# Optimization experiments

Measured on AMD Instinct MI355X. Metric: run time of the kernel, lower is better.

## Reference

```python
import jax, jax.numpy as jnp
import numpy as np

POOLSCALE = 4  # HSA: avg-pool kernel/stride = (scale, scale*4)

def _avg_pool(x, kh, kw):
    # kernel == stride and dims divisible -> exact reshape-mean pooling
    B, C, H, W = x.shape
    return x.reshape(B, C, H // kh, kh, W // kw, kw).mean(axis=(3, 5))

def setup_inputs() -> dict:
    key = jax.random.key(0)
    k1, k2, k3 = jax.random.split(key, 3)
    shape = (4, 64, 192, 192)
    return {
        "K": jax.random.normal(k1, shape, dtype=jnp.float32),
        "Q": jax.random.normal(k2, shape, dtype=jnp.float32),
        "V": jax.random.normal(k3, shape, dtype=jnp.float32),
    }

def reference(K, Q, V):
    B, C, H, W = Q.shape
    kh, kw = POOLSCALE, POOLSCALE * 4
    Qp = Q.reshape(B, C, H * W).transpose(0, 2, 1)          # [B, HW, C]
    Kp = _avg_pool(K, kh, kw)                               # [B, C, h, w]
    Kp = Kp.reshape(B, C, -1)                               # [B, C, hw_p]
    Vp = _avg_pool(V, kh, kw).reshape(B, C, -1)             # [B, C, hw_p]
    scores = jnp.einsum('bnc,bcm->bnm', Qp, Kp)             # [B, HW, hw_p]
    attn = jax.nn.softmax(scores, axis=1)                   # softmax over query dim (dim=1), as in torch code
    out = jnp.einsum('bcm,bnm->bcn', Vp, attn)              # V_pie @ attn^T -> [B, C, HW]
    return out.reshape(B, C, H, W)
```

## Files before the change

kernel.cpp:

```cpp
#include <hip/hip_runtime.h>
#include <stdint.h>

#define BB 4
#define CC 64
#define HH 192
#define WW 192
#define HWN (HH*WW)
#define KH 4
#define KW 16
#define PW (WW/KW)
#define MP ((HH/KH)*(WW/KW))
#define MITER (MP/64)
#define NCHUNK (HWN/256)
#define NBTOT (HWN/32)
#define SCALE_W 65536.0f
#define INV_SCALE (1.0f/65536.0f)

typedef _Float16 half8 __attribute__((ext_vector_type(8)));
typedef _Float16 half4 __attribute__((ext_vector_type(4)));
typedef float floatx4 __attribute__((ext_vector_type(4)));

static __device__ __forceinline__ void gload16(const void* g, void* l) {
  __builtin_amdgcn_global_load_lds((const __attribute__((address_space(1))) void*)g,
                                   (__attribute__((address_space(3))) void*)l, 16, 0, 0);
}
#define WAITCNT_VM(N) asm volatile("s_waitcnt vmcnt(" #N ")" ::: "memory")
#define WAITCNT_LGKM0 asm volatile("s_waitcnt lgkmcnt(0)" ::: "memory")


__global__ __launch_bounds__(256) void pool_kernel(
    const float* __restrict__ Kin, const float* __restrict__ Vin,
    _Float16* __restrict__ kptF, float* __restrict__ vp) {
  int t = blockIdx.x * 256 + threadIdx.x;
  const int total = BB * CC * MP;
  bool isV = t >= total;
  int idx = isV ? t - total : t;
  int m = idx % MP;
  int c = (idx / MP) % CC;
  int b = idx / (MP * CC);
  int mh = m / PW, mw = m % PW;
  const float* src = (isV ? Vin : Kin) + (((b * CC + c) * HH + mh * KH) * WW + mw * KW);
  float s = 0.f;
#pragma unroll
  for (int r = 0; r < KH; ++r) {
    const float4* row = (const float4*)(src + r * WW);
#pragma unroll
    for (int j = 0; j < KW / 4; ++j) {
      float4 v = row[j];
      s += v.x + v.y + v.z + v.w;
    }
  }
  s *= (1.0f / (KH * KW));
  if (isV) {
    vp[(b * CC + c) * MP + m] = s;
  } else {
    int mi = m >> 6, mloc = m & 63, l15 = mloc >> 2, mf = mloc & 3;
    int ks = c >> 5, lhi = (c >> 3) & 3, e = c & 7;
    int lane = lhi * 16 + l15;
    kptF[(((((b * MITER + mi) * 4 + mf) * 2 + ks)) * 64 + lane) * 8 + e] = (_Float16)s;
  }
}

__global__ __launch_bounds__(256) void qprep_kernel(
    const float* __restrict__ Q, _Float16* __restrict__ qF) {
  int t = blockIdx.x * 256 + threadIdx.x;
  int chunk = t >> 6;
  int lane = t & 63;
  int nf = chunk & 1;
  int ks = (chunk >> 1) & 1;
  int idx = chunk >> 2;
  int nb = idx % NBTOT;
  int b = idx / NBTOT;
  int c0 = ks * 32 + (lane >> 4) * 8;
  int n = nb * 32 + nf * 16 + (lane & 15);
  const float* Qb = Q + (b * CC + c0) * HWN + n;
  half8 h;
#pragma unroll
  for (int e = 0; e < 8; ++e) h[e] = (_Float16)Qb[e * HWN];
  *(half8*)(qF + chunk * 512 + lane * 8) = h;
}

__global__ __launch_bounds__(512) void colsum_qf_kernel(
    const _Float16* __restrict__ qF, const _Float16* __restrict__ kptF,
    float* __restrict__ part) {
  int tid = threadIdx.x;
  int lane = tid & 63;
  int l15 = lane & 15;
  int u = blockIdx.x * 8 + (tid >> 6);
  int mi = u % 9;
  int v = u / 9;
  int b = v / NCHUNK;
  int nc = v % NCHUNK;

  const _Float16* kb = kptF + b * MITER * 8 * 512;
  half8 bfr[4][2];
#pragma unroll
  for (int mf = 0; mf < 4; ++mf)
#pragma unroll
    for (int ks = 0; ks < 2; ++ks)
      bfr[mf][ks] = *(const half8*)(kb + ((mi * 4 + mf) * 2 + ks) * 512 + lane * 8);

  floatx4 zero = {0.f, 0.f, 0.f, 0.f};
  float s0 = 0.f, s1 = 0.f, s2 = 0.f, s3 = 0.f;

#pragma unroll
  for (int it = 0; it < 8; ++it) {
    int nb = nc * 8 + it;
    const _Float16* qc = qF + (size_t)((b * NBTOT + nb) * 4) * 512 + lane * 8;
    half8 af[2][2];
#pragma unroll
    for (int ks = 0; ks < 2; ++ks)
#pragma unroll
      for (int nf = 0; nf < 2; ++nf)
        af[nf][ks] = *(const half8*)(qc + (ks * 2 + nf) * 512);

    floatx4 sacc[2][4];
#pragma unroll
    for (int nf = 0; nf < 2; ++nf)
#pragma unroll
      for (int mf = 0; mf < 4; ++mf) sacc[nf][mf] = zero;
    __builtin_amdgcn_s_setprio(1);
#pragma unroll
    for (int ks = 0; ks < 2; ++ks)
#pragma unroll
      for (int nf = 0; nf < 2; ++nf)
#pragma unroll
        for (int mf = 0; mf < 4; ++mf)
          sacc[nf][mf] = __builtin_amdgcn_mfma_f32_16x16x32_f16(
              af[nf][ks], bfr[mf][ks], sacc[nf][mf], 0, 0, 0);
    __builtin_amdgcn_s_setprio(0);

#pragma unroll
    for (int nf = 0; nf < 2; ++nf)
#pragma unroll
      for (int r = 0; r < 4; ++r) {
        s0 += __expf(sacc[nf][0][r]);
        s1 += __expf(sacc[nf][1][r]);
        s2 += __expf(sacc[nf][2][r]);
        s3 += __expf(sacc[nf][3][r]);
      }
  }

  s0 += __shfl_xor(s0, 16); s0 += __shfl_xor(s0, 32);
  s1 += __shfl_xor(s1, 16); s1 += __shfl_xor(s1, 32);
  s2 += __shfl_xor(s2, 16); s2 += __shfl_xor(s2, 32);
  s3 += __shfl_xor(s3, 16); s3 += __shfl_xor(s3, 32);
  if (lane < 16) {
    float* p = part + (b * NCHUNK + nc) * MP + mi * 64 + l15 * 4;
    p[0] = s0; p[1] = s1; p[2] = s2; p[3] = s3;
  }
}

__global__ __launch_bounds__(576) void colsum_fb_kernel(
    const float* __restrict__ Q, const _Float16* __restrict__ kptF,
    float* __restrict__ part) {
  int b = blockIdx.y;
  int n0 = blockIdx.x * 256;
  int tid = threadIdx.x;
  int wv = tid / 64;
  int lane = tid & 63;
  int l15 = lane & 15, lhi = lane >> 4;

  const _Float16* kb = kptF + b * MITER * 8 * 512;
  half8 bfr[4][2];
#pragma unroll
  for (int mf = 0; mf < 4; ++mf)
#pragma unroll
    for (int ks = 0; ks < 2; ++ks)
      bfr[mf][ks] = *(const half8*)(kb + ((wv * 4 + mf) * 2 + ks) * 512 + lane * 8);

  const float* Qb = Q + b * CC * HWN;
  floatx4 zero = {0.f, 0.f, 0.f, 0.f};
  float s0 = 0.f, s1 = 0.f, s2 = 0.f, s3 = 0.f;

#pragma unroll
  for (int it = 0; it < 8; ++it) {
    int nr = n0 + it * 32 + l15;
    half8 af[2][2];
#pragma unroll
    for (int nf = 0; nf < 2; ++nf)
#pragma unroll
      for (int ks = 0; ks < 2; ++ks)
#pragma unroll
        for (int e = 0; e < 8; ++e)
          af[nf][ks][e] = (_Float16)Qb[(ks * 32 + lhi * 8 + e) * HWN + nr + nf * 16];

    floatx4 sacc[2][4];
#pragma unroll
    for (int nf = 0; nf < 2; ++nf)
#pragma unroll
      for (int mf = 0; mf < 4; ++mf) sacc[nf][mf] = zero;
    __builtin_amdgcn_s_setprio(1);
#pragma unroll
    for (int ks = 0; ks < 2; ++ks)
#pragma unroll
      for (int nf = 0; nf < 2; ++nf)
#pragma unroll
        for (int mf = 0; mf < 4; ++mf)
          sacc[nf][mf] = __builtin_amdgcn_mfma_f32_16x16x32_f16(
              af[nf][ks], bfr[mf][ks], sacc[nf][mf], 0, 0, 0);
    __builtin_amdgcn_s_setprio(0);

#pragma unroll
    for (int nf = 0; nf < 2; ++nf)
#pragma unroll
      for (int r = 0; r < 4; ++r) {
        s0 += __expf(sacc[nf][0][r]);
        s1 += __expf(sacc[nf][1][r]);
        s2 += __expf(sacc[nf][2][r]);
        s3 += __expf(sacc[nf][3][r]);
      }
  }

  s0 += __shfl_xor(s0, 16); s0 += __shfl_xor(s0, 32);
  s1 += __shfl_xor(s1, 16); s1 += __shfl_xor(s1, 32);
  s2 += __shfl_xor(s2, 16); s2 += __shfl_xor(s2, 32);
  s3 += __shfl_xor(s3, 16); s3 += __shfl_xor(s3, 32);
  if (lane < 16) {
    float* p = part + (b * NCHUNK + blockIdx.x) * MP + wv * 64 + l15 * 4;
    p[0] = s0; p[1] = s1; p[2] = s2; p[3] = s3;
  }
}

__global__ __launch_bounds__(256) void colsum_reduce_kernel(
    const float* __restrict__ part, float* __restrict__ colsum) {
  int t = blockIdx.x * 256 + threadIdx.x;
  int m = t % MP;
  int b = t / MP;
  const float* p = part + b * NCHUNK * MP + m;
  float a0 = 0.f, a1 = 0.f, a2 = 0.f, a3 = 0.f;
#pragma unroll 4
  for (int nc = 0; nc < NCHUNK; nc += 4) {
    a0 += p[(nc + 0) * MP];
    a1 += p[(nc + 1) * MP];
    a2 += p[(nc + 2) * MP];
    a3 += p[(nc + 3) * MP];
  }
  colsum[t] = (a0 + a1) + (a2 + a3);
}

__global__ __launch_bounds__(256) void wprep_kernel(
    const float* __restrict__ vp, const float* __restrict__ colsum,
    _Float16* __restrict__ wqF) {
  int t = blockIdx.x * 256 + threadIdx.x;
  int m = t % MP;
  int c = (t / MP) % CC;
  int b = t / (CC * MP);
  float w = vp[t] / colsum[b * MP + m] * SCALE_W;
  int cf = c >> 4, l15 = c & 15;
  int mi = m >> 6, mloc = m & 63;
  int ks = mloc >> 5, lhi = (mloc >> 3) & 3, e = mloc & 7;
  int lane = lhi * 16 + l15;
  wqF[((((b * MITER + mi) * 4 + cf) * 2 + ks) * 64 + lane) * 8 + e] = (_Float16)w;
}

__global__ __launch_bounds__(256, 2) void attn_main_kernel(
    const float* __restrict__ Q, const _Float16* __restrict__ kptF,
    const _Float16* __restrict__ wqF, float* __restrict__ out) {
  __shared__ char lds[3 * 16384 + 4 * 4096];
  char* stg = lds;
  int b = blockIdx.y;
  int n0 = blockIdx.x * 128;
  int tid = threadIdx.x;
  int wv = tid >> 6;
  int lane = tid & 63;
  int l15 = lane & 15, lhi = lane >> 4;
  char* eb = lds + 49152 + wv * 4096;

  const _Float16* kb = kptF + b * MITER * 8 * 512;
  const _Float16* wb = wqF + b * MITER * 8 * 512;

#define STAGE_A(tt, ss)                                                        \
  {                                                                            \
    int q0_ = wv * 4;                                                          \
    _Pragma("unroll") for (int j_ = 0; j_ < 4; ++j_) {                         \
      int q_ = q0_ + j_;                                                       \
      const _Float16* sp_ = (q_ < 8 ? kb + (tt) * 4096 + q_ * 512              \
                                    : wb + (tt) * 4096 + (q_ - 8) * 512) +     \
                            lane * 8;                                          \
      gload16(sp_, stg + (ss) * 16384 + q_ * 1024);                            \
    }                                                                          \
  }

  STAGE_A(0, 0);
  STAGE_A(1, 1);

  const float* Qb = Q + b * CC * HWN;
  int nrow = n0 + wv * 32 + l15;
  half8 afrag[2][2];
#pragma unroll
  for (int nf = 0; nf < 2; ++nf)
#pragma unroll
    for (int ks = 0; ks < 2; ++ks)
#pragma unroll
      for (int e = 0; e < 8; ++e)
        afrag[nf][ks][e] = (_Float16)Qb[(ks * 32 + lhi * 8 + e) * HWN + nrow + nf * 16];

  floatx4 zero = {0.f, 0.f, 0.f, 0.f};
  floatx4 oacc[4][2];
#pragma unroll
  for (int cf = 0; cf < 4; ++cf)
#pragma unroll
    for (int nf = 0; nf < 2; ++nf) oacc[cf][nf] = zero;

  WAITCNT_VM(4);
  __builtin_amdgcn_sched_barrier(0);
  __builtin_amdgcn_s_barrier();

#pragma unroll
  for (int mi = 0; mi < MITER; ++mi) {
    const int sc = mi % 3;
    const int spv = (mi + 2) % 3;

    if (mi >= 1) {
      if (mi <= 7) { WAITCNT_VM(4); } else { WAITCNT_VM(0); }
      __builtin_amdgcn_sched_barrier(0);
      __builtin_amdgcn_s_barrier();
    }

    half8 bfr[4][2];
#pragma unroll
    for (int mf = 0; mf < 4; ++mf)
#pragma unroll
      for (int ks = 0; ks < 2; ++ks)
        bfr[mf][ks] = *(const half8*)(stg + sc * 16384 + (mf * 2 + ks) * 1024 + lane * 16);
    half8 wfr[4][2];
    half8 ef[2][2];
    if (mi >= 1) {
#pragma unroll
      for (int cf = 0; cf < 4; ++cf)
#pragma unroll
        for (int ks = 0; ks < 2; ++ks)
          wfr[cf][ks] = *(const half8*)(stg + spv * 16384 + 8192 + (cf * 2 + ks) * 1024 + lane * 16);
#pragma unroll
      for (int nf = 0; nf < 2; ++nf)
#pragma unroll
        for (int ks = 0; ks < 2; ++ks) {
          int nl = nf * 16 + l15;
          int slot = (ks * 4 + lhi) ^ (nl & 7);
          ef[nf][ks] = *(const half8*)(eb + nl * 128 + (slot << 4));
        }
    }

    WAITCNT_LGKM0;
    __builtin_amdgcn_sched_barrier(0);
    __builtin_amdgcn_s_barrier();

    if (mi + 2 < MITER) STAGE_A(mi + 2, spv);

    floatx4 sacc[2][4];
#pragma unroll
    for (int nf = 0; nf < 2; ++nf)
#pragma unroll
      for (int mf = 0; mf < 4; ++mf) sacc[nf][mf] = zero;
    __builtin_amdgcn_s_setprio(1);
#pragma unroll
    for (int ks = 0; ks < 2; ++ks)
#pragma unroll
      for (int nf = 0; nf < 2; ++nf)
#pragma unroll
        for (int mf = 0; mf < 4; ++mf)
          sacc[nf][mf] = __builtin_amdgcn_mfma_f32_16x16x32_f16(
              afrag[nf][ks], bfr[mf][ks], sacc[nf][mf], 0, 0, 0);
    if (mi >= 1) {
#pragma unroll
      for (int ks = 0; ks < 2; ++ks)
#pragma unroll
        for (int cf = 0; cf < 4; ++cf)
#pragma unroll
          for (int nf = 0; nf < 2; ++nf)
            oacc[cf][nf] = __builtin_amdgcn_mfma_f32_16x16x32_f16(
                wfr[cf][ks], ef[nf][ks], oacc[cf][nf], 0, 0, 0);
    }
    __builtin_amdgcn_s_setprio(0);

#pragma unroll
    for (int nf = 0; nf < 2; ++nf)
#pragma unroll
      for (int r = 0; r < 4; ++r) {
        int nl = nf * 16 + lhi * 4 + r;
        half4 h;
#pragma unroll
        for (int mf = 0; mf < 4; ++mf) h[mf] = (_Float16)__expf(sacc[nf][mf][r]);
        int byte = nl * 128 + ((((l15 >> 1) ^ (nl & 7))) << 4) + ((l15 & 1) << 3);
        *(half4*)(eb + byte) = h;
      }
  }

  {
    half8 wfr[4][2];
#pragma unroll
    for (int cf = 0; cf < 4; ++cf)
#pragma unroll
      for (int ks = 0; ks < 2; ++ks)
        wfr[cf][ks] = *(const half8*)(stg + 2 * 16384 + 8192 + (cf * 2 + ks) * 1024 + lane * 16);
    half8 ef[2][2];
#pragma unroll
    for (int nf = 0; nf < 2; ++nf)
#pragma unroll
      for (int ks = 0; ks < 2; ++ks) {
        int nl = nf * 16 + l15;
        int slot = (ks * 4 + lhi) ^ (nl & 7);
        ef[nf][ks] = *(const half8*)(eb + nl * 128 + (slot << 4));
      }
    __builtin_amdgcn_s_setprio(1);
#pragma unroll
    for (int ks = 0; ks < 2; ++ks)
#pragma unroll
      for (int cf = 0; cf < 4; ++cf)
#pragma unroll
        for (int nf = 0; nf < 2; ++nf)
          oacc[cf][nf] = __builtin_amdgcn_mfma_f32_16x16x32_f16(
              wfr[cf][ks], ef[nf][ks], oacc[cf][nf], 0, 0, 0);
    __builtin_amdgcn_s_setprio(0);
  }

  float* ob = out + b * CC * HWN;
#pragma unroll
  for (int cf = 0; cf < 4; ++cf)
#pragma unroll
    for (int nf = 0; nf < 2; ++nf)
#pragma unroll
      for (int r = 0; r < 4; ++r) {
        int c = cf * 16 + lhi * 4 + r;
        int n = n0 + wv * 32 + nf * 16 + l15;
        ob[c * HWN + n] = oacc[cf][nf][r] * INV_SCALE;
      }
}

extern "C" void kernel_launch(void* const* d_in, const int* in_sizes, int n_in,
                              void* d_out, int out_size, void* d_ws, size_t ws_size,
                              hipStream_t stream) {
  const float* K = (const float*)d_in[0];
  const float* Q = (const float*)d_in[1];
  const float* V = (const float*)d_in[2];
  float* out = (float*)d_out;
  char* ws = (char*)d_ws;
  _Float16* kptF  = (_Float16*)(ws);
  float*    vp    = (float*)(ws + 294912);
  _Float16* wqF   = (_Float16*)(ws + 294912 + 589824);
  float*    colsum = (float*)(ws + 294912 + 589824 + 294912);
  const size_t QF_OFF = 1204224;
  const size_t QF_BYTES = (size_t)BB * NBTOT * 4 * 512 * 2;
  _Float16* qF = (_Float16*)(ws + QF_OFF);
  float* part = out;

  pool_kernel<<<(2 * BB * CC * MP) / 256, 256, 0, stream>>>(K, V, kptF, vp);
  if (ws_size >= QF_OFF + QF_BYTES) {
    qprep_kernel<<<(BB * NBTOT * 4 * 64) / 256, 256, 0, stream>>>(Q, qF);
    colsum_qf_kernel<<<(BB * NCHUNK * 9) / 8, 512, 0, stream>>>(qF, kptF, part);
  } else {
    colsum_fb_kernel<<<dim3(NCHUNK, BB), 576, 0, stream>>>(Q, kptF, part);
  }
  colsum_reduce_kernel<<<(BB * MP) / 256, 256, 0, stream>>>(part, colsum);
  wprep_kernel<<<(BB * CC * MP) / 256, 256, 0, stream>>>(vp, colsum, wqF);
  attn_main_kernel<<<dim3(HWN / 128, BB), 256, 0, stream>>>(Q, kptF, wqF, out);
}
```

Baseline: 88.37 us.

## Add attention kernel reading pre-packed fp16 Q fragments instead of fp32 Q

Adds attn_qf_kernel, which loads Q from the fp16 MFMA-fragment buffer already produced by qprep instead of re-reading and converting fp32 Q. It also shrinks staging to a double buffer and tiles 32 queries per wave, giving 128 per block. Each wave keeps its own Q fragments in registers across all key iterations. The main attention kernel should read half the Q bytes and skip the conversion work, at the cost of a different occupancy and tiling profile. The fp32 path remains as a fallback when the workspace is too small.

New measurement: 85.55 us. -3.2%, faster.

```diff
diff --git a/kernel.cpp b/kernel.cpp
--- a/kernel.cpp
+++ b/kernel.cpp
@@ -252,6 +252,135 @@
   int ks = mloc >> 5, lhi = (mloc >> 3) & 3, e = mloc & 7;
   int lane = lhi * 16 + l15;
   wqF[((((b * MITER + mi) * 4 + cf) * 2 + ks) * 64 + lane) * 8 + e] = (_Float16)w;
+}
+
+__global__ __launch_bounds__(256) void attn_qf_kernel(
+    const _Float16* __restrict__ qF, const _Float16* __restrict__ kptF,
+    const _Float16* __restrict__ wqF, float* __restrict__ out) {
+  __shared__ char lds[2 * 16384 + 4 * 4096];
+  char* stg = lds;
+  int b = blockIdx.y;
+  int tid = threadIdx.x;
+  int wv = tid >> 6;
+  int lane = tid & 63;
+  int l15 = lane & 15, lhi = lane >> 4;
+  char* eb = lds + 32768 + wv * 4096;
+
+  const _Float16* kb = kptF + b * MITER * 8 * 512;
+  const _Float16* wb = wqF + b * MITER * 8 * 512;
+
+#define STAGE_Q(tt, ss)                                                        \
+  {                                                                            \
+    int q0_ = wv * 4;                                                          \
+    _Pragma("unroll") for (int j_ = 0; j_ < 4; ++j_) {                         \
+      int q_ = q0_ + j_;                                                       \
+      const _Float16* sp_ = (q_ < 8 ? kb + (tt) * 4096 + q_ * 512              \
+                                    : wb + (tt) * 4096 + (q_ - 8) * 512) +     \
+                            lane * 8;                                          \
+      gload16(sp_, stg + (ss) * 16384 + q_ * 1024);                            \
+    }                                                                          \
+  }
+
+  STAGE_Q(0, 0);
+
+  int nb = blockIdx.x * 4 + wv;
+  const _Float16* qc = qF + (size_t)((b * NBTOT + nb) * 4) * 512 + lane * 8;
+  half8 afrag[2][2];
+#pragma unroll
+  for (int ks = 0; ks < 2; ++ks)
+#pragma unroll
+    for (int nf = 0; nf < 2; ++nf)
+      afrag[nf][ks] = *(const half8*)(qc + (ks * 2 + nf) * 512);
+
+  floatx4 zero = {0.f, 0.f, 0.f, 0.f};
+  floatx4 oacc[4][2];
+#pragma unroll
+  for (int cf = 0; cf < 4; ++cf)
+#pragma unroll
+    for (int nf = 0; nf < 2; ++nf) oacc[cf][nf] = zero;
+
+#pragma unroll
+  for (int mi = 0; mi < MITER; ++mi) {
+    const int sc = mi & 1;
+    WAITCNT_LGKM0;
+    WAITCNT_VM(0);
+    __builtin_amdgcn_sched_barrier(0);
+    __builtin_amdgcn_s_barrier();
+    if (mi + 1 < MITER) STAGE_Q(mi + 1, sc ^ 1);
+
+    half8 bfr[4][2];
+#pragma unroll
+    for (int mf = 0; mf < 4; ++mf)
+#pragma unroll
+      for (int ks = 0; ks < 2; ++ks)
+        bfr[mf][ks] = *(const half8*)(stg + sc * 16384 + (mf * 2 + ks) * 1024 + lane * 16);
+    half8 wfr[4][2];
+#pragma unroll
+    for (int cf = 0; cf < 4; ++cf)
+#pragma unroll
+      for (int ks = 0; ks < 2; ++ks)
+        wfr[cf][ks] = *(const half8*)(stg + sc * 16384 + 8192 + (cf * 2 + ks) * 1024 + lane * 16);
+
+    floatx4 sacc[2][4];
+#pragma unroll
+    for (int nf = 0; nf < 2; ++nf)
+#pragma unroll
+      for (int mf = 0; mf < 4; ++mf) sacc[nf][mf] = zero;
+    __builtin_amdgcn_s_setprio(1);
+#pragma unroll
+    for (int ks = 0; ks < 2; ++ks)
+#pragma unroll
+      for (int nf = 0; nf < 2; ++nf)
+#pragma unroll
+        for (int mf = 0; mf < 4; ++mf)
+          sacc[nf][mf] = __builtin_amdgcn_mfma_f32_16x16x32_f16(
+              afrag[nf][ks], bfr[mf][ks], sacc[nf][mf], 0, 0, 0);
+    __builtin_amdgcn_s_setprio(0);
+
+#pragma unroll
+    for (int nf = 0; nf < 2; ++nf)
+#pragma unroll
+      for (int r = 0; r < 4; ++r) {
+        int nl = nf * 16 + lhi * 4 + r;
+        half4 h;
+#pragma unroll
+        for (int mf = 0; mf < 4; ++mf) h[mf] = (_Float16)__expf(sacc[nf][mf][r]);
+        int byte = nl * 128 + ((((l15 >> 1) ^ (nl & 7))) << 4) + ((l15 & 1) << 3);
+        *(half4*)(eb + byte) = h;
+      }
+
+    half8 ef[2][2];
+#pragma unroll
+    for (int nf = 0; nf < 2; ++nf)
+#pragma unroll
+      for (int ks = 0; ks < 2; ++ks) {
+        int nl = nf * 16 + l15;
+        int slot = (ks * 4 + lhi) ^ (nl & 7);
+        ef[nf][ks] = *(const half8*)(eb + nl * 128 + (slot << 4));
+      }
+    __builtin_amdgcn_s_setprio(1);
+#pragma unroll
+    for (int ks = 0; ks < 2; ++ks)
+#pragma unroll
+      for (int cf = 0; cf < 4; ++cf)
+#pragma unroll
+        for (int nf = 0; nf < 2; ++nf)
+          oacc[cf][nf] = __builtin_amdgcn_mfma_f32_16x16x32_f16(
+              wfr[cf][ks], ef[nf][ks], oacc[cf][nf], 0, 0, 0);
+    __builtin_amdgcn_s_setprio(0);
+  }
+
+  float* ob = out + b * CC * HWN;
+#pragma unroll
+  for (int cf = 0; cf < 4; ++cf)
+#pragma unroll
+    for (int nf = 0; nf < 2; ++nf)
+#pragma unroll
+      for (int r = 0; r < 4; ++r) {
+        int c = cf * 16 + lhi * 4 + r;
+        int n = nb * 32 + nf * 16 + l15;
+        ob[c * HWN + n] = oacc[cf][nf][r] * INV_SCALE;
+      }
 }
 
 __global__ __launch_bounds__(256, 2) void attn_main_kernel(
@@ -449,10 +578,13 @@
   if (ws_size >= QF_OFF + QF_BYTES) {
     qprep_kernel<<<(BB * NBTOT * 4 * 64) / 256, 256, 0, stream>>>(Q, qF);
     colsum_qf_kernel<<<(BB * NCHUNK * 9) / 8, 512, 0, stream>>>(qF, kptF, part);
+    colsum_reduce_kernel<<<(BB * MP) / 256, 256, 0, stream>>>(part, colsum);
+    wprep_kernel<<<(BB * CC * MP) / 256, 256, 0, stream>>>(vp, colsum, wqF);
+    attn_qf_kernel<<<dim3(NBTOT / 4, BB), 256, 0, stream>>>(qF, kptF, wqF, out);
   } else {
     colsum_fb_kernel<<<dim3(NCHUNK, BB), 576, 0, stream>>>(Q, kptF, part);
-  }
-  colsum_reduce_kernel<<<(BB * MP) / 256, 256, 0, stream>>>(part, colsum);
-  wprep_kernel<<<(BB * CC * MP) / 256, 256, 0, stream>>>(vp, colsum, wqF);
-  attn_main_kernel<<<dim3(HWN / 128, BB), 256, 0, stream>>>(Q, kptF, wqF, out);
-}
+    colsum_reduce_kernel<<<(BB * MP) / 256, 256, 0, stream>>>(part, colsum);
+    wprep_kernel<<<(BB * CC * MP) / 256, 256, 0, stream>>>(vp, colsum, wqF);
+    attn_main_kernel<<<dim3(HWN / 128, BB), 256, 0, stream>>>(Q, kptF, wqF, out);
+  }
+}
```
